# Performance work log

Hardware: AMD Instinct MI355X
Metric: run time of the kernel (lower is better)

## Reference

```python
import jax, jax.numpy as jnp
import numpy as np

N, E, B = 50000, 800000, 64      # nodes, edges, graphs per branch
F_IN, C = 128, 128               # input feats, convolution_neurons
H = 2                            # hidden_layers
EPS = 1e-3                       # keras BatchNormalization epsilon


def _gconv(x, src, dst, W, b, gamma, beta):
    # Spektral GeneralConv: linear -> gather(src) -> scatter-sum(dst) -> BN(inference, mean=0,var=1) -> relu
    h = x @ W + b                                            # [N, C]
    agg = jax.ops.segment_sum(h[src], dst, num_segments=x.shape[0])  # [N, C]
    agg = agg * (gamma / np.float32(np.sqrt(1.0 + EPS))) + beta
    return jax.nn.relu(agg)


def _avg_pool(x, seg):
    s = jax.ops.segment_sum(x, seg, num_segments=B)          # [B, C]
    cnt = jax.ops.segment_sum(jnp.ones((x.shape[0],), x.dtype), seg, num_segments=B)
    return s / jnp.maximum(cnt, 1.0)[:, None]


def setup_inputs() -> dict:
    key = jax.random.key(0)
    ks = jax.random.split(key, 12)

    def glorot(k, shp):
        lim = float(np.sqrt(6.0 / (shp[0] + shp[1])))
        return jax.random.uniform(k, shp, jnp.float32, -lim, lim)

    inp = {}
    inp["x1"] = jax.random.normal(ks[0], (N, F_IN), jnp.float32)
    inp["x2"] = jax.random.normal(ks[1], (N, F_IN), jnp.float32)
    inp["edges1"] = jax.random.randint(ks[2], (2, E), 0, N)
    inp["edges2"] = jax.random.randint(ks[3], (2, E), 0, N)
    inp["seg1"] = jnp.sort(jax.random.randint(ks[4], (N,), 0, B))
    inp["seg2"] = jnp.sort(jax.random.randint(ks[5], (N,), 0, B))
    # branch 1: GeneralConv(128) then GeneralConv(64)
    inp["W1a"], inp["b1a"] = glorot(ks[6], (F_IN, C)), jnp.zeros((C,), jnp.float32)
    inp["g1a"], inp["be1a"] = jnp.ones((C,), jnp.float32), jnp.zeros((C,), jnp.float32)
    inp["W1b"], inp["b1b"] = glorot(ks[7], (C, C // 2)), jnp.zeros((C // 2,), jnp.float32)
    inp["g1b"], inp["be1b"] = jnp.ones((C // 2,), jnp.float32), jnp.zeros((C // 2,), jnp.float32)
    # branch 2
    inp["W2a"], inp["b2a"] = glorot(ks[8], (F_IN, C)), jnp.zeros((C,), jnp.float32)
    inp["g2a"], inp["be2a"] = jnp.ones((C,), jnp.float32), jnp.zeros((C,), jnp.float32)
    inp["W2b"], inp["b2b"] = glorot(ks[9], (C, C // 2)), jnp.zeros((C // 2,), jnp.float32)
    inp["g2b"], inp["be2b"] = jnp.ones((C // 2,), jnp.float32), jnp.zeros((C // 2,), jnp.float32)
    # shared hidden dense + output head
    inp["Wd"], inp["bd"] = glorot(ks[10], (C, C)), jnp.zeros((C,), jnp.float32)
    inp["Wo"], inp["bo"] = glorot(ks[11], (C, 1)), jnp.zeros((1,), jnp.float32)
    return inp


def reference(x1, x2, edges1, edges2, seg1, seg2,
              W1a, b1a, g1a, be1a, W1b, b1b, g1b, be1b,
              W2a, b2a, g2a, be2a, W2b, b2b, g2b, be2b,
              Wd, bd, Wo, bo):
    h1 = _gconv(x1, edges1[0], edges1[1], W1a, b1a, g1a, be1a)   # [N, 128]
    h1 = _gconv(h1, edges1[0], edges1[1], W1b, b1b, g1b, be1b)   # [N, 64]
    p1 = _avg_pool(h1, seg1)                                      # [B, 64]
    h2 = _gconv(x2, edges2[0], edges2[1], W2a, b2a, g2a, be2a)
    h2 = _gconv(h2, edges2[0], edges2[1], W2b, b2b, g2b, be2b)
    p2 = _avg_pool(h2, seg2)
    out = jnp.concatenate([p1, p2], axis=-1)                      # [B, 128]
    for _ in range(H):  # shared Dense(128, relu) applied hidden_layers times
        out = jax.nn.relu(out @ Wd + bd)
    return jax.nn.sigmoid(out @ Wo + bo)                          # [B, 1]
```

## Files before the change

### kernel.cpp

```cpp
#include <hip/hip_runtime.h>
#include <math.h>

#define GS    512
#define GSH   9
#define NGMAX 128
#define FCAP  48
#define SCAP  10240


__global__ __launch_bounds__(1024) void bin_kernel(
    const int* __restrict__ s1, const int* __restrict__ d1,
    const int* __restrict__ s2, const int* __restrict__ d2,
    int* __restrict__ gcur, int* __restrict__ pairs, int E, int G1) {
  __shared__ int fifo[NGMAX][FCAP];
  __shared__ int fcnt[NGMAX];
  __shared__ int fbase[NGMAX];
  __shared__ int fpre[NGMAX + 1];
  const int* src = blockIdx.y ? s2 : s1;
  const int* dst = blockIdx.y ? d2 : d1;
  int gboff = blockIdx.y * G1;
  int tid = threadIdx.x;
  if (tid < NGMAX) fcnt[tid] = 0;
  __syncthreads();
  int e0 = blockIdx.x * 4096;
  for (int r = 0; r < 4; ++r) {
    int e = e0 + r * 1024 + tid;
    if (e < E) {
      int s = src[e], d = dst[e];
      int g = d >> GSH;
      int pk = s | ((d & (GS - 1)) << 17);
      int pos = atomicAdd(&fcnt[g], 1);
      if (pos < FCAP) fifo[g][pos] = pk;
      else {
        int gp = atomicAdd(&gcur[gboff + g], 1);
        pairs[(size_t)(gboff + g) * SCAP + gp] = pk;
      }
    }
    __syncthreads();
    if (tid < G1) {
      int c = fcnt[tid];
      if (c > FCAP) c = FCAP;
      fcnt[tid] = c;
      fbase[tid] = (c > 0) ? atomicAdd(&gcur[gboff + tid], c) : 0;
    }
    __syncthreads();
    if (tid == 0) {
      int acc = 0;
      for (int i = 0; i < G1; ++i) { fpre[i] = acc; acc += fcnt[i]; }
      fpre[G1] = acc;
    }
    __syncthreads();
    int T = fpre[G1];
    for (int t = tid; t < T; t += 1024) {
      int lo = 0, hi = G1;
      while (hi - lo > 1) { int mid = (lo + hi) >> 1; if (fpre[mid] <= t) lo = mid; else hi = mid; }
      int idx = t - fpre[lo];
      pairs[(size_t)(gboff + lo) * SCAP + fbase[lo] + idx] = fifo[lo][idx];
    }
    __syncthreads();
    if (tid < NGMAX) fcnt[tid] = 0;
    __syncthreads();
  }
}


__global__ __launch_bounds__(1024) void refine_kernel(
    const int* __restrict__ gcur, int* __restrict__ pairs,
    int* __restrict__ offs, int* __restrict__ counts, int N, int G1) {
  __shared__ int stg[SCAP];
  __shared__ int hist[GS];
  __shared__ int excl[GS];
  __shared__ int wtot[8];
  int gl = blockIdx.x, br = blockIdx.y;
  int g = br * G1 + gl;
  size_t rbase = (size_t)g * SCAP;
  int rcnt = gcur[g];
  if (rcnt > SCAP) rcnt = SCAP;
  int tid = threadIdx.x;
  if (tid < GS) hist[tid] = 0;
  __syncthreads();
  for (int i = tid; i < rcnt; i += 1024) {
    int pk = pairs[rbase + i];
    stg[i] = pk;
    atomicAdd(&hist[pk >> 17], 1);
  }
  __syncthreads();
  if (tid < GS) {
    int lane = tid & 63, wv = tid >> 6;
    int v = hist[tid];
    int inc = v;
    #pragma unroll
    for (int off = 1; off < 64; off <<= 1) {
      int t = __shfl_up(inc, off);
      if (lane >= off) inc += t;
    }
    excl[tid] = inc - v;
    if (lane == 63) wtot[wv] = inc;
  }
  __syncthreads();
  if (tid == 0) {
    int a = 0;
    #pragma unroll
    for (int w = 0; w < 8; ++w) { int t = wtot[w]; wtot[w] = a; a += t; }
  }
  __syncthreads();
  if (tid < GS) excl[tid] += wtot[tid >> 6];
  __syncthreads();
  int node0 = gl * GS;
  int nloc = N - node0; if (nloc > GS) nloc = GS;
  for (int j = tid; j < nloc; j += 1024) {
    offs[br * N + node0 + j] = (int)rbase + excl[j];
    counts[br * N + node0 + j] = hist[j];
  }
  __syncthreads();
  for (int i = tid; i < rcnt; i += 1024) {
    int pk = stg[i];
    int pos = atomicAdd(&excl[pk >> 17], 1);
    pairs[rbase + pos] = pk & 0x1FFFF;
  }
}


template <int COUT>
__global__ __launch_bounds__(256, 2) void gemm_kernel(const float* __restrict__ X,
                                                      const float* __restrict__ W,
                                                      const float* __restrict__ bias,
                                                      float* __restrict__ Y, int nrows) {
  constexpr int CG = COUT / 4;
  constexpr int RG = 256 / CG;
  constexpr int BM = 64;
  constexpr int RPT = BM / RG;
  __shared__ float xs[BM][132];
  int tid = threadIdx.x;
  int block_row = blockIdx.x * BM;
  for (int i = tid; i < BM * 32; i += 256) {
    int r = i >> 5, c4 = i & 31;
    int gr = block_row + r;
    float4 v = make_float4(0.f, 0.f, 0.f, 0.f);
    if (gr < nrows) v = reinterpret_cast<const float4*>(X + (size_t)gr * 128)[c4];
    *reinterpret_cast<float4*>(&xs[r][c4 * 4]) = v;
  }
  __syncthreads();
  int c0 = (tid % CG) * 4;
  int r0 = (tid / CG) * RPT;
  float acc[RPT][4] = {};
  #pragma unroll 2
  for (int k = 0; k < 128; k += 4) {
    float4 w0 = *reinterpret_cast<const float4*>(&W[(k + 0) * COUT + c0]);
    float4 w1 = *reinterpret_cast<const float4*>(&W[(k + 1) * COUT + c0]);
    float4 w2 = *reinterpret_cast<const float4*>(&W[(k + 2) * COUT + c0]);
    float4 w3 = *reinterpret_cast<const float4*>(&W[(k + 3) * COUT + c0]);
    #pragma unroll
    for (int i = 0; i < RPT; ++i) {
      float4 x = *reinterpret_cast<const float4*>(&xs[r0 + i][k]);
      acc[i][0] = fmaf(x.x, w0.x, acc[i][0]);
      acc[i][1] = fmaf(x.x, w0.y, acc[i][1]);
      acc[i][2] = fmaf(x.x, w0.z, acc[i][2]);
      acc[i][3] = fmaf(x.x, w0.w, acc[i][3]);
      acc[i][0] = fmaf(x.y, w1.x, acc[i][0]);
      acc[i][1] = fmaf(x.y, w1.y, acc[i][1]);
      acc[i][2] = fmaf(x.y, w1.z, acc[i][2]);
      acc[i][3] = fmaf(x.y, w1.w, acc[i][3]);
      acc[i][0] = fmaf(x.z, w2.x, acc[i][0]);
      acc[i][1] = fmaf(x.z, w2.y, acc[i][1]);
      acc[i][2] = fmaf(x.z, w2.z, acc[i][2]);
      acc[i][3] = fmaf(x.z, w2.w, acc[i][3]);
      acc[i][0] = fmaf(x.w, w3.x, acc[i][0]);
      acc[i][1] = fmaf(x.w, w3.y, acc[i][1]);
      acc[i][2] = fmaf(x.w, w3.z, acc[i][2]);
      acc[i][3] = fmaf(x.w, w3.w, acc[i][3]);
    }
  }
  float4 bv = *reinterpret_cast<const float4*>(&bias[c0]);
  #pragma unroll
  for (int i = 0; i < RPT; ++i) {
    int gr = block_row + r0 + i;
    if (gr < nrows) {
      float4 o;
      o.x = acc[i][0] + bv.x; o.y = acc[i][1] + bv.y;
      o.z = acc[i][2] + bv.z; o.w = acc[i][3] + bv.w;
      *reinterpret_cast<float4*>(&Y[(size_t)gr * COUT + c0]) = o;
    }
  }
}


template <int C>
__global__ __launch_bounds__(256) void agg_kernel(const float* __restrict__ h,
                                                  const int* __restrict__ offs,
                                                  const int* __restrict__ counts,
                                                  const int* __restrict__ csr_src,
                                                  const float* __restrict__ gamma,
                                                  const float* __restrict__ beta,
                                                  float* __restrict__ out, int n) {
  int node = blockIdx.x * 4 + (threadIdx.x >> 6);
  if (node >= n) return;
  node = __builtin_amdgcn_readfirstlane(node);
  int lane = threadIdx.x & 63;
  int half = lane >> 5;
  int l5 = lane & 31;
  int beg = offs[node], cnt = counts[node];
  const int* lp = csr_src + beg;
  float a0 = 0.f, a1 = 0.f, a2 = 0.f, a3 = 0.f;
  for (int base = 0; base < cnt; base += 64) {
    int rem = cnt - base;
    int m = rem < 64 ? rem : 64;
    int idx = lp[base + (lane < m ? lane : m - 1)];
    int mfull = m & ~15;
    int j = 0;
    for (; j < mfull; j += 16) {
      if (C == 128) {
        float4 v[8];
        #pragma unroll
        for (int u = 0; u < 8; ++u) {
          int s = __shfl(idx, j + 2 * u + half);
          v[u] = *reinterpret_cast<const float4*>(h + (size_t)s * 128 + l5 * 4);
        }
        #pragma unroll
        for (int u = 0; u < 8; ++u) { a0 += v[u].x; a1 += v[u].y; a2 += v[u].z; a3 += v[u].w; }
      } else {
        float2 v[8];
        #pragma unroll
        for (int u = 0; u < 8; ++u) {
          int s = __shfl(idx, j + 2 * u + half);
          v[u] = *reinterpret_cast<const float2*>(h + (size_t)s * 64 + l5 * 2);
        }
        #pragma unroll
        for (int u = 0; u < 8; ++u) { a0 += v[u].x; a1 += v[u].y; }
      }
    }
    if (j < m) {
      if (C == 128) {
        float4 v[8];
        #pragma unroll
        for (int u = 0; u < 8; ++u) {
          int ed = j + 2 * u + half;
          int s = __shfl(idx, ed < m ? ed : m - 1);
          v[u] = *reinterpret_cast<const float4*>(h + (size_t)s * 128 + l5 * 4);
        }
        #pragma unroll
        for (int u = 0; u < 8; ++u) {
          bool ok = (j + 2 * u + half) < m;
          a0 += ok ? v[u].x : 0.f;
          a1 += ok ? v[u].y : 0.f;
          a2 += ok ? v[u].z : 0.f;
          a3 += ok ? v[u].w : 0.f;
        }
      } else {
        float2 v[8];
        #pragma unroll
        for (int u = 0; u < 8; ++u) {
          int ed = j + 2 * u + half;
          int s = __shfl(idx, ed < m ? ed : m - 1);
          v[u] = *reinterpret_cast<const float2*>(h + (size_t)s * 64 + l5 * 2);
        }
        #pragma unroll
        for (int u = 0; u < 8; ++u) {
          bool ok = (j + 2 * u + half) < m;
          a0 += ok ? v[u].x : 0.f;
          a1 += ok ? v[u].y : 0.f;
        }
      }
    }
  }
  a0 += __shfl_xor(a0, 32);
  a1 += __shfl_xor(a1, 32);
  if (C == 128) { a2 += __shfl_xor(a2, 32); a3 += __shfl_xor(a3, 32); }
  const float inv = 1.0f / sqrtf(1.0f + 1.0e-3f);
  if (half == 0) {
    if (C == 128) {
      float4 g = reinterpret_cast<const float4*>(gamma)[l5];
      float4 b = reinterpret_cast<const float4*>(beta)[l5];
      float4 o;
      o.x = fmaxf(fmaf(a0, g.x * inv, b.x), 0.f);
      o.y = fmaxf(fmaf(a1, g.y * inv, b.y), 0.f);
      o.z = fmaxf(fmaf(a2, g.z * inv, b.z), 0.f);
      o.w = fmaxf(fmaf(a3, g.w * inv, b.w), 0.f);
      *reinterpret_cast<float4*>(out + (size_t)node * 128 + l5 * 4) = o;
    } else {
      float2 g = reinterpret_cast<const float2*>(gamma)[l5];
      float2 b = reinterpret_cast<const float2*>(beta)[l5];
      float2 o;
      o.x = fmaxf(fmaf(a0, g.x * inv, b.x), 0.f);
      o.y = fmaxf(fmaf(a1, g.y * inv, b.y), 0.f);
      *reinterpret_cast<float2*>(out + (size_t)node * 64 + l5 * 2) = o;
    }
  }
}


__global__ __launch_bounds__(1024) void pool_kernel(const float* __restrict__ h,
                                                    const int* __restrict__ seg,
                                                    float* __restrict__ p, int n) {
  int g = blockIdx.x;
  int lo, hi;
  { int l = 0, r = n; while (l < r) { int m = (l + r) >> 1; if (seg[m] < g) l = m + 1; else r = m; } lo = l; }
  { int l = 0, r = n; while (l < r) { int m = (l + r) >> 1; if (seg[m] < g + 1) l = m + 1; else r = m; } hi = l; }
  int c = threadIdx.x & 63;
  int sub = threadIdx.x >> 6;
  float acc = 0.f;
  for (int i = lo + sub; i < hi; i += 16) acc += h[(size_t)i * 64 + c];
  __shared__ float red[16][64];
  red[sub][c] = acc;
  __syncthreads();
  if (sub == 0) {
    float s = 0.f;
    #pragma unroll
    for (int k = 0; k < 16; ++k) s += red[k][c];
    float cnt = (float)(hi - lo);
    p[g * 64 + c] = s / fmaxf(cnt, 1.0f);
  }
}


__global__ __launch_bounds__(512) void head_kernel(const float* __restrict__ p,
                                                   const float* __restrict__ Wd,
                                                   const float* __restrict__ bd,
                                                   const float* __restrict__ Wo,
                                                   const float* __restrict__ bo,
                                                   float* __restrict__ out) {
  __shared__ float cur[64][128];
  __shared__ float nxt[64][128];
  int tid = threadIdx.x;
  const float* p1 = p;
  const float* p2 = p + 64 * 64;
  for (int i = tid; i < 64 * 128; i += 512) {
    int r = i >> 7, c = i & 127;
    cur[r][c] = (c < 64) ? p1[r * 64 + c] : p2[r * 64 + (c - 64)];
  }
  __syncthreads();
  int c0 = (tid & 31) * 4;
  int r0 = (tid >> 5) * 4;
  for (int layer = 0; layer < 2; ++layer) {
    float acc[4][4] = {};
    #pragma unroll 4
    for (int k = 0; k < 128; ++k) {
      float4 w = *reinterpret_cast<const float4*>(&Wd[k * 128 + c0]);
      #pragma unroll
      for (int i = 0; i < 4; ++i) {
        float x = cur[r0 + i][k];
        acc[i][0] = fmaf(x, w.x, acc[i][0]);
        acc[i][1] = fmaf(x, w.y, acc[i][1]);
        acc[i][2] = fmaf(x, w.z, acc[i][2]);
        acc[i][3] = fmaf(x, w.w, acc[i][3]);
      }
    }
    float4 bv = *reinterpret_cast<const float4*>(&bd[c0]);
    __syncthreads();
    #pragma unroll
    for (int i = 0; i < 4; ++i) {
      float4 o;
      o.x = fmaxf(acc[i][0] + bv.x, 0.f);
      o.y = fmaxf(acc[i][1] + bv.y, 0.f);
      o.z = fmaxf(acc[i][2] + bv.z, 0.f);
      o.w = fmaxf(acc[i][3] + bv.w, 0.f);
      *reinterpret_cast<float4*>(&nxt[r0 + i][c0]) = o;
    }
    __syncthreads();
    for (int i = tid; i < 64 * 128; i += 512) (&cur[0][0])[i] = (&nxt[0][0])[i];
    __syncthreads();
  }
  int wv = tid >> 6, lane = tid & 63;
  for (int r = wv; r < 64; r += 8) {
    float v = cur[r][lane] * Wo[lane] + cur[r][64 + lane] * Wo[64 + lane];
    #pragma unroll
    for (int off = 32; off; off >>= 1) v += __shfl_down(v, off);
    if (lane == 0) out[r] = 1.0f / (1.0f + expf(-(v + bo[0])));
  }
}


extern "C" void kernel_launch(void* const* d_in, const int* in_sizes, int n_in,
                              void* d_out, int out_size, void* d_ws, size_t ws_size,
                              hipStream_t stream) {
  const float* x1  = (const float*)d_in[0];
  const float* x2  = (const float*)d_in[1];
  const int* e1    = (const int*)d_in[2];
  const int* e2    = (const int*)d_in[3];
  const int* seg1  = (const int*)d_in[4];
  const int* seg2  = (const int*)d_in[5];
  const float* W1a = (const float*)d_in[6];  const float* b1a = (const float*)d_in[7];
  const float* g1a = (const float*)d_in[8];  const float* be1a = (const float*)d_in[9];
  const float* W1b = (const float*)d_in[10]; const float* b1b = (const float*)d_in[11];
  const float* g1b = (const float*)d_in[12]; const float* be1b = (const float*)d_in[13];
  const float* W2a = (const float*)d_in[14]; const float* b2a = (const float*)d_in[15];
  const float* g2a = (const float*)d_in[16]; const float* be2a = (const float*)d_in[17];
  const float* W2b = (const float*)d_in[18]; const float* b2b = (const float*)d_in[19];
  const float* g2b = (const float*)d_in[20]; const float* be2b = (const float*)d_in[21];
  const float* Wd  = (const float*)d_in[22]; const float* bd  = (const float*)d_in[23];
  const float* Wo  = (const float*)d_in[24]; const float* bo  = (const float*)d_in[25];
  float* out = (float*)d_out;

  const int N = in_sizes[0] / 128;
  const int E = in_sizes[2] / 2;
  const int G1 = (N + GS - 1) >> GSH;
  const int G  = 2 * G1;

  char* ws = (char*)d_ws;
  size_t off = 0;
  auto alloc = [&](size_t bytes) -> void* {
    void* ptr = ws + off;
    off += (bytes + 255) & ~(size_t)255;
    return ptr;
  };
  float* h    = (float*)alloc((size_t)N * 128 * sizeof(float));
  float* aggb = (float*)alloc((size_t)N * 128 * sizeof(float));
  int* pairs  = (int*)alloc((size_t)G * SCAP * sizeof(int));
  int* offs   = (int*)alloc((size_t)(2 * N) * sizeof(int));
  int* counts = (int*)alloc((size_t)(2 * N) * sizeof(int));
  int* gcur   = (int*)alloc((size_t)(G + 8) * sizeof(int));
  float* pbuf = (float*)alloc(2 * 64 * 64 * sizeof(float));
  (void)ws_size; (void)n_in; (void)out_size;

  hipMemsetAsync(gcur, 0, (size_t)(G + 8) * sizeof(int), stream);
  {
    dim3 gb((E + 4095) / 4096, 2);
    bin_kernel<<<gb, 1024, 0, stream>>>(e1, e1 + E, e2, e2 + E, gcur, pairs, E, G1);
    dim3 gr(G1, 2);
    refine_kernel<<<gr, 1024, 0, stream>>>(gcur, pairs, offs, counts, N, G1);
  }

  struct Branch {
    const float *x; const int *seg;
    const float *Wa, *ba, *ga, *bea, *Wb, *bb, *gb, *beb;
  };
  Branch brs[2] = {
    {x1, seg1, W1a, b1a, g1a, be1a, W1b, b1b, g1b, be1b},
    {x2, seg2, W2a, b2a, g2a, be2a, W2b, b2b, g2b, be2b},
  };

  for (int b = 0; b < 2; ++b) {
    const int* offs_b = offs + b * N;
    const int* cnts_b = counts + b * N;
    gemm_kernel<128><<<(N + 63) / 64, 256, 0, stream>>>(brs[b].x, brs[b].Wa, brs[b].ba, h, N);
    agg_kernel<128><<<(N + 3) / 4, 256, 0, stream>>>(h, offs_b, cnts_b, pairs, brs[b].ga, brs[b].bea, aggb, N);
    gemm_kernel<64><<<(N + 63) / 64, 256, 0, stream>>>(aggb, brs[b].Wb, brs[b].bb, h, N);
    agg_kernel<64><<<(N + 3) / 4, 256, 0, stream>>>(h, offs_b, cnts_b, pairs, brs[b].gb, brs[b].beb, aggb, N);
    pool_kernel<<<64, 1024, 0, stream>>>(aggb, brs[b].seg, pbuf + b * 64 * 64, N);
  }
  head_kernel<<<1, 512, 0, stream>>>(pbuf, Wd, bd, Wo, bo, out);
}
```

Measured before the change: 380.1 us.

## Batch both branches per launch and split 128-channel aggregation into 64-channel halves

The GEMM and pooling kernels now process both graph branches in a single launch through a second grid dimension, which halves their launch count and fills more of the GPU per launch. The 128-wide aggregation is split so that each block gathers only one 64-channel half of every neighbour row. This shrinks the per-half working set of the gathered features, which should raise cache hit rates on the random-index gathers. The cost is that edge indices are read and shuffled twice, and separate buffers per branch use more workspace.

```diff
diff --git a/kernel.cpp b/kernel.cpp
--- a/kernel.cpp
+++ b/kernel.cpp
@@ -122,14 +122,19 @@
 
 
 template <int COUT>
-__global__ __launch_bounds__(256, 2) void gemm_kernel(const float* __restrict__ X,
-                                                      const float* __restrict__ W,
-                                                      const float* __restrict__ bias,
-                                                      float* __restrict__ Y, int nrows) {
+__global__ __launch_bounds__(256, 2) void gemm2_kernel(
+    const float* __restrict__ X0, const float* __restrict__ X1,
+    const float* __restrict__ W0, const float* __restrict__ W1,
+    const float* __restrict__ bias0, const float* __restrict__ bias1,
+    float* __restrict__ Y0, float* __restrict__ Y1, int nrows) {
   constexpr int CG = COUT / 4;
   constexpr int RG = 256 / CG;
   constexpr int BM = 64;
   constexpr int RPT = BM / RG;
+  const float* X = blockIdx.y ? X1 : X0;
+  const float* W = blockIdx.y ? W1 : W0;
+  const float* bias = blockIdx.y ? bias1 : bias0;
+  float* Y = blockIdx.y ? Y1 : Y0;
   __shared__ float xs[BM][132];
   int tid = threadIdx.x;
   int block_row = blockIdx.x * BM;
@@ -185,14 +190,73 @@
 }
 
 
-template <int C>
-__global__ __launch_bounds__(256) void agg_kernel(const float* __restrict__ h,
-                                                  const int* __restrict__ offs,
-                                                  const int* __restrict__ counts,
-                                                  const int* __restrict__ csr_src,
-                                                  const float* __restrict__ gamma,
-                                                  const float* __restrict__ beta,
-                                                  float* __restrict__ out, int n) {
+__global__ __launch_bounds__(256) void agg128_kernel(
+    const float* __restrict__ h, const int* __restrict__ offs,
+    const int* __restrict__ counts, const int* __restrict__ csr_src,
+    const float* __restrict__ gamma, const float* __restrict__ beta,
+    float* __restrict__ out, int n) {
+  int node = blockIdx.x * 4 + (threadIdx.x >> 6);
+  if (node >= n) return;
+  node = __builtin_amdgcn_readfirstlane(node);
+  int ch = blockIdx.y;
+  int lane = threadIdx.x & 63;
+  int half = lane >> 5;
+  int l5 = lane & 31;
+  const float* hh = h + ch * 64;
+  int beg = offs[node], cnt = counts[node];
+  const int* lp = csr_src + beg;
+  float a0 = 0.f, a1 = 0.f;
+  for (int base = 0; base < cnt; base += 64) {
+    int rem = cnt - base;
+    int m = rem < 64 ? rem : 64;
+    int idx = lp[base + (lane < m ? lane : m - 1)];
+    int mfull = m & ~15;
+    int j = 0;
+    for (; j < mfull; j += 16) {
+      float2 v[8];
+      #pragma unroll
+      for (int u = 0; u < 8; ++u) {
+        int s = __shfl(idx, j + 2 * u + half);
+        v[u] = *reinterpret_cast<const float2*>(hh + (size_t)s * 128 + l5 * 2);
+      }
+      #pragma unroll
+      for (int u = 0; u < 8; ++u) { a0 += v[u].x; a1 += v[u].y; }
+    }
+    if (j < m) {
+      float2 v[8];
+      #pragma unroll
+      for (int u = 0; u < 8; ++u) {
+        int ed = j + 2 * u + half;
+        int s = __shfl(idx, ed < m ? ed : m - 1);
+        v[u] = *reinterpret_cast<const float2*>(hh + (size_t)s * 128 + l5 * 2);
+      }
+      #pragma unroll
+      for (int u = 0; u < 8; ++u) {
+        bool ok = (j + 2 * u + half) < m;
+        a0 += ok ? v[u].x : 0.f;
+        a1 += ok ? v[u].y : 0.f;
+      }
+    }
+  }
+  a0 += __shfl_xor(a0, 32);
+  a1 += __shfl_xor(a1, 32);
+  const float inv = 1.0f / sqrtf(1.0f + 1.0e-3f);
+  if (half == 0) {
+    float2 g = reinterpret_cast<const float2*>(gamma + ch * 64)[l5];
+    float2 b = reinterpret_cast<const float2*>(beta + ch * 64)[l5];
+    float2 o;
+    o.x = fmaxf(fmaf(a0, g.x * inv, b.x), 0.f);
+    o.y = fmaxf(fmaf(a1, g.y * inv, b.y), 0.f);
+    *reinterpret_cast<float2*>(out + (size_t)node * 128 + ch * 64 + l5 * 2) = o;
+  }
+}
+
+
+__global__ __launch_bounds__(256) void agg64_kernel(
+    const float* __restrict__ h, const int* __restrict__ offs,
+    const int* __restrict__ counts, const int* __restrict__ csr_src,
+    const float* __restrict__ gamma, const float* __restrict__ beta,
+    float* __restrict__ out, int n) {
   int node = blockIdx.x * 4 + (threadIdx.x >> 6);
   if (node >= n) return;
   node = __builtin_amdgcn_readfirstlane(node);
@@ -201,7 +265,7 @@
   int l5 = lane & 31;
   int beg = offs[node], cnt = counts[node];
   const int* lp = csr_src + beg;
-  float a0 = 0.f, a1 = 0.f, a2 = 0.f, a3 = 0.f;
+  float a0 = 0.f, a1 = 0.f;
   for (int base = 0; base < cnt; base += 64) {
     int rem = cnt - base;
     int m = rem < 64 ? rem : 64;
@@ -209,89 +273,52 @@
     int mfull = m & ~15;
     int j = 0;
     for (; j < mfull; j += 16) {
-      if (C == 128) {
-        float4 v[8];
-        #pragma unroll
-        for (int u = 0; u < 8; ++u) {
-          int s = __shfl(idx, j + 2 * u + half);
-          v[u] = *reinterpret_cast<const float4*>(h + (size_t)s * 128 + l5 * 4);
-        }
-        #pragma unroll
-        for (int u = 0; u < 8; ++u) { a0 += v[u].x; a1 += v[u].y; a2 += v[u].z; a3 += v[u].w; }
-      } else {
-        float2 v[8];
-        #pragma unroll
-        for (int u = 0; u < 8; ++u) {
-          int s = __shfl(idx, j + 2 * u + half);
-          v[u] = *reinterpret_cast<const float2*>(h + (size_t)s * 64 + l5 * 2);
-        }
-        #pragma unroll
-        for (int u = 0; u < 8; ++u) { a0 += v[u].x; a1 += v[u].y; }
-      }
+      float2 v[8];
+      #pragma unroll
+      for (int u = 0; u < 8; ++u) {
+        int s = __shfl(idx, j + 2 * u + half);
+        v[u] = *reinterpret_cast<const float2*>(h + (size_t)s * 64 + l5 * 2);
+      }
+      #pragma unroll
+      for (int u = 0; u < 8; ++u) { a0 += v[u].x; a1 += v[u].y; }
     }
     if (j < m) {
-      if (C == 128) {
-        float4 v[8];
-        #pragma unroll
-        for (int u = 0; u < 8; ++u) {
-          int ed = j + 2 * u + half;
-          int s = __shfl(idx, ed < m ? ed : m - 1);
-          v[u] = *reinterpret_cast<const float4*>(h + (size_t)s * 128 + l5 * 4);
-        }
-        #pragma unroll
-        for (int u = 0; u < 8; ++u) {
-          bool ok = (j + 2 * u + half) < m;
-          a0 += ok ? v[u].x : 0.f;
-          a1 += ok ? v[u].y : 0.f;
-          a2 += ok ? v[u].z : 0.f;
-          a3 += ok ? v[u].w : 0.f;
-        }
-      } else {
-        float2 v[8];
-        #pragma unroll
-        for (int u = 0; u < 8; ++u) {
-          int ed = j + 2 * u + half;
-          int s = __shfl(idx, ed < m ? ed : m - 1);
-          v[u] = *reinterpret_cast<const float2*>(h + (size_t)s * 64 + l5 * 2);
-        }
-        #pragma unroll
-        for (int u = 0; u < 8; ++u) {
-          bool ok = (j + 2 * u + half) < m;
-          a0 += ok ? v[u].x : 0.f;
-          a1 += ok ? v[u].y : 0.f;
-        }
+      float2 v[8];
+      #pragma unroll
+      for (int u = 0; u < 8; ++u) {
+        int ed = j + 2 * u + half;
+        int s = __shfl(idx, ed < m ? ed : m - 1);
+        v[u] = *reinterpret_cast<const float2*>(h + (size_t)s * 64 + l5 * 2);
+      }
+      #pragma unroll
+      for (int u = 0; u < 8; ++u) {
+        bool ok = (j + 2 * u + half) < m;
+        a0 += ok ? v[u].x : 0.f;
+        a1 += ok ? v[u].y : 0.f;
       }
     }
   }
   a0 += __shfl_xor(a0, 32);
   a1 += __shfl_xor(a1, 32);
-  if (C == 128) { a2 += __shfl_xor(a2, 32); a3 += __shfl_xor(a3, 32); }
   const float inv = 1.0f / sqrtf(1.0f + 1.0e-3f);
   if (half == 0) {
-    if (C == 128) {
-      float4 g = reinterpret_cast<const float4*>(gamma)[l5];
-      float4 b = reinterpret_cast<const float4*>(beta)[l5];
-      float4 o;
-      o.x = fmaxf(fmaf(a0, g.x * inv, b.x), 0.f);
-      o.y = fmaxf(fmaf(a1, g.y * inv, b.y), 0.f);
-      o.z = fmaxf(fmaf(a2, g.z * inv, b.z), 0.f);
-      o.w = fmaxf(fmaf(a3, g.w * inv, b.w), 0.f);
-      *reinterpret_cast<float4*>(out + (size_t)node * 128 + l5 * 4) = o;
-    } else {
-      float2 g = reinterpret_cast<const float2*>(gamma)[l5];
-      float2 b = reinterpret_cast<const float2*>(beta)[l5];
-      float2 o;
-      o.x = fmaxf(fmaf(a0, g.x * inv, b.x), 0.f);
-      o.y = fmaxf(fmaf(a1, g.y * inv, b.y), 0.f);
-      *reinterpret_cast<float2*>(out + (size_t)node * 64 + l5 * 2) = o;
-    }
-  }
-}
-
-
-__global__ __launch_bounds__(1024) void pool_kernel(const float* __restrict__ h,
-                                                    const int* __restrict__ seg,
-                                                    float* __restrict__ p, int n) {
+    float2 g = reinterpret_cast<const float2*>(gamma)[l5];
+    float2 b = reinterpret_cast<const float2*>(beta)[l5];
+    float2 o;
+    o.x = fmaxf(fmaf(a0, g.x * inv, b.x), 0.f);
+    o.y = fmaxf(fmaf(a1, g.y * inv, b.y), 0.f);
+    *reinterpret_cast<float2*>(out + (size_t)node * 64 + l5 * 2) = o;
+  }
+}
+
+
+__global__ __launch_bounds__(1024) void pool2_kernel(
+    const float* __restrict__ h0, const float* __restrict__ h1,
+    const int* __restrict__ seg0, const int* __restrict__ seg1,
+    float* __restrict__ p, int n) {
+  const float* h = blockIdx.y ? h1 : h0;
+  const int* seg = blockIdx.y ? seg1 : seg0;
+  float* pb = p + blockIdx.y * 64 * 64;
   int g = blockIdx.x;
   int lo, hi;
   { int l = 0, r = n; while (l < r) { int m = (l + r) >> 1; if (seg[m] < g) l = m + 1; else r = m; } lo = l; }
@@ -308,7 +335,7 @@
     #pragma unroll
     for (int k = 0; k < 16; ++k) s += red[k][c];
     float cnt = (float)(hi - lo);
-    p[g * 64 + c] = s / fmaxf(cnt, 1.0f);
+    pb[g * 64 + c] = s / fmaxf(cnt, 1.0f);
   }
 }
 
@@ -403,8 +430,10 @@
     off += (bytes + 255) & ~(size_t)255;
     return ptr;
   };
-  float* h    = (float*)alloc((size_t)N * 128 * sizeof(float));
-  float* aggb = (float*)alloc((size_t)N * 128 * sizeof(float));
+  float* h0   = (float*)alloc((size_t)N * 128 * sizeof(float));
+  float* h1   = (float*)alloc((size_t)N * 128 * sizeof(float));
+  float* ag0  = (float*)alloc((size_t)N * 128 * sizeof(float));
+  float* ag1  = (float*)alloc((size_t)N * 128 * sizeof(float));
   int* pairs  = (int*)alloc((size_t)G * SCAP * sizeof(int));
   int* offs   = (int*)alloc((size_t)(2 * N) * sizeof(int));
   int* counts = (int*)alloc((size_t)(2 * N) * sizeof(int));
@@ -420,23 +449,27 @@
     refine_kernel<<<gr, 1024, 0, stream>>>(gcur, pairs, offs, counts, N, G1);
   }
 
-  struct Branch {
-    const float *x; const int *seg;
-    const float *Wa, *ba, *ga, *bea, *Wb, *bb, *gb, *beb;
-  };
-  Branch brs[2] = {
-    {x1, seg1, W1a, b1a, g1a, be1a, W1b, b1b, g1b, be1b},
-    {x2, seg2, W2a, b2a, g2a, be2a, W2b, b2b, g2b, be2b},
-  };
-
-  for (int b = 0; b < 2; ++b) {
-    const int* offs_b = offs + b * N;
-    const int* cnts_b = counts + b * N;
-    gemm_kernel<128><<<(N + 63) / 64, 256, 0, stream>>>(brs[b].x, brs[b].Wa, brs[b].ba, h, N);
-    agg_kernel<128><<<(N + 3) / 4, 256, 0, stream>>>(h, offs_b, cnts_b, pairs, brs[b].ga, brs[b].bea, aggb, N);
-    gemm_kernel<64><<<(N + 63) / 64, 256, 0, stream>>>(aggb, brs[b].Wb, brs[b].bb, h, N);
-    agg_kernel<64><<<(N + 3) / 4, 256, 0, stream>>>(h, offs_b, cnts_b, pairs, brs[b].gb, brs[b].beb, aggb, N);
-    pool_kernel<<<64, 1024, 0, stream>>>(aggb, brs[b].seg, pbuf + b * 64 * 64, N);
+  const int* offs0 = offs;       const int* cnts0 = counts;
+  const int* offs1 = offs + N;   const int* cnts1 = counts + N;
+
+  {
+    dim3 gg((N + 63) / 64, 2);
+    gemm2_kernel<128><<<gg, 256, 0, stream>>>(x1, x2, W1a, W2a, b1a, b2a, h0, h1, N);
+  }
+  {
+    dim3 ga((N + 3) / 4, 2);
+    agg128_kernel<<<ga, 256, 0, stream>>>(h0, offs0, cnts0, pairs, g1a, be1a, ag0, N);
+    agg128_kernel<<<ga, 256, 0, stream>>>(h1, offs1, cnts1, pairs, g2a, be2a, ag1, N);
+  }
+  {
+    dim3 gg((N + 63) / 64, 2);
+    gemm2_kernel<64><<<gg, 256, 0, stream>>>(ag0, ag1, W1b, W2b, b1b, b2b, h0, h1, N);
+  }
+  agg64_kernel<<<(N + 3) / 4, 256, 0, stream>>>(h0, offs0, cnts0, pairs, g1b, be1b, ag0, N);
+  agg64_kernel<<<(N + 3) / 4, 256, 0, stream>>>(h1, offs1, cnts1, pairs, g2b, be2b, ag1, N);
+  {
+    dim3 gp(64, 2);
+    pool2_kernel<<<gp, 1024, 0, stream>>>(ag0, ag1, seg1, seg2, pbuf, N);
   }
   head_kernel<<<1, 512, 0, stream>>>(pbuf, Wd, bd, Wo, bo, out);
 }
```

After: 336.6 us. 1.13x faster.
